# Performance work log

Measured on AMD Instinct MI355X. Metric: run time of the kernel, lower is better.

The kernel has to match this reference:

```python
import jax, jax.numpy as jnp
import numpy as np

N = 262144
IN_DIM = 64
HID = 256
EMB = 128
OUT = 64
B = 16
MAX_AISLES = 64
NUM_SEG = B * MAX_AISLES  # static upper bound on number of (batch, aisle) segments


def setup_inputs() -> dict:
    key = jax.random.key(0)
    ks = jax.random.split(key, 16)
    def lin(k, fan_in, fan_out):
        bound = 1.0 / np.sqrt(fan_in)
        kw, kb = jax.random.split(k)
        W = jax.random.uniform(kw, (fan_in, fan_out), jnp.float32, -bound, bound)
        b = jax.random.uniform(kb, (fan_out,), jnp.float32, -bound, bound)
        return W, b
    W1, b1 = lin(ks[0], IN_DIM, HID)
    W2, b2 = lin(ks[1], HID, HID)
    W3, b3 = lin(ks[2], HID, EMB)
    A1, c1 = lin(ks[3], 2 * EMB, HID)
    A2, c2 = lin(ks[4], HID, HID)
    A3, c3 = lin(ks[5], HID, OUT)
    x = jax.random.normal(ks[6], (N, IN_DIM), jnp.float32)
    aisle_nrs = jax.random.randint(ks[7], (N,), 0, MAX_AISLES, jnp.int32)
    batch = jnp.sort(jax.random.randint(ks[8], (N,), 0, B, jnp.int32))
    return {"x": x, "aisle_nrs": aisle_nrs, "batch": batch,
            "W1": W1, "b1": b1, "W2": W2, "b2": b2, "W3": W3, "b3": b3,
            "A1": A1, "c1": c1, "A2": A2, "c2": c2, "A3": A3, "c3": c3}


def reference(x, aisle_nrs, batch, W1, b1, W2, b2, W3, b3, A1, c1, A2, c2, A3, c3):
    lrelu = lambda v: jax.nn.leaky_relu(v, 0.01)  # torch LeakyReLU default slope
    h = lrelu(x @ W1 + b1)
    h = lrelu(h @ W2 + b2)
    h = h @ W3 + b3  # [N, EMB]
    # dynamic group id: aisle + batch * (max_aisle + 1)
    aisle_ids = aisle_nrs + batch * (jnp.max(aisle_nrs) + 1)
    # scatter-mean over segments (NUM_SEG is a static upper bound)
    sums = jax.ops.segment_sum(h, aisle_ids, num_segments=NUM_SEG)
    counts = jax.ops.segment_sum(jnp.ones((h.shape[0],), h.dtype), aisle_ids,
                                 num_segments=NUM_SEG)
    means = sums / jnp.maximum(counts, 1.0)[:, None]
    # gather back and concat
    z = jnp.concatenate([h, means[aisle_ids]], axis=1)  # [N, 2*EMB]
    z = lrelu(z @ A1 + c1)
    z = lrelu(z @ A2 + c2)
    z = z @ A3 + c3
    return z
```

## Files before the change

### kernel.cpp

```cpp
#include <hip/hip_runtime.h>
#include <hip/hip_bf16.h>

#define N_ROWS 262144
#define IN_DIM 64
#define HID 256
#define EMB 128
#define OUT_DIM 64
#define NSEG 1024
#define ROWS_B 128
#define MT 8
#define NWAVE 8
#define LDS_S 264
#define CHUNK 1024
#define NSLOTS (2 * (N_ROWS / CHUNK))

typedef _Float16 h16;
typedef _Float16 h16x8 __attribute__((ext_vector_type(8)));
typedef _Float16 h16x4 __attribute__((ext_vector_type(4)));
typedef float f32x4 __attribute__((ext_vector_type(4)));


__global__ void k_max(const int* __restrict__ aisle, int* __restrict__ maxA) {
    int v = 0;
    for (int i = blockIdx.x * blockDim.x + threadIdx.x; i < N_ROWS; i += gridDim.x * blockDim.x)
        v = max(v, aisle[i]);
#pragma unroll
    for (int off = 32; off > 0; off >>= 1) v = max(v, __shfl_down(v, off));
    __shared__ int red[4];
    if ((threadIdx.x & 63) == 0) red[threadIdx.x >> 6] = v;
    __syncthreads();
    if (threadIdx.x == 0) {
        int m = red[0];
        for (int i = 1; i < 4; ++i) m = max(m, red[i]);
        atomicMax(maxA, m);
    }
}

__device__ __forceinline__ void frag_nk(int o, int K, int& n, int& k) {
    int tile = o / (16 * K);
    int r = o - tile * 16 * K;
    n = tile * 16 + ((r >> 3) & 15);
    k = (r >> 9) * 32 + (((r >> 7) & 3) << 3) + (r & 7);
}

__global__ void k_prep_weights(const float* __restrict__ W1, const float* __restrict__ W2,
                               const float* __restrict__ W3, const float* __restrict__ A1f,
                               const float* __restrict__ A2f, const float* __restrict__ A3f,
                               h16* __restrict__ W1t, h16* __restrict__ W2t, h16* __restrict__ W3t,
                               h16* __restrict__ A1t, h16* __restrict__ A2t, h16* __restrict__ A3t) {
    int idx = blockIdx.x * 256 + threadIdx.x;
    int n, k;
    if (idx < 16384)       { int o = idx;          frag_nk(o, 64, n, k);  W1t[o] = (h16)W1[k * 256 + n]; }
    else if (idx < 81920)  { int o = idx - 16384;  frag_nk(o, 256, n, k); W2t[o] = (h16)W2[k * 256 + n]; }
    else if (idx < 114688) { int o = idx - 81920;  frag_nk(o, 256, n, k); W3t[o] = (h16)W3[k * 128 + n]; }
    else if (idx < 180224) { int o = idx - 114688; frag_nk(o, 256, n, k); A1t[o] = (h16)A1f[k * 256 + n]; }
    else if (idx < 245760) { int o = idx - 180224; frag_nk(o, 256, n, k); A2t[o] = (h16)A2f[k * 256 + n]; }
    else                   { int o = idx - 245760; frag_nk(o, 256, n, k); A3t[o] = (h16)A3f[k * 64  + n]; }
}

template <int K, int NOUT, bool ACT>
__device__ __forceinline__ void mlp_layer_ip(const h16* __restrict__ Wt,
                                             const float* __restrict__ bias,
                                             h16* __restrict__ S,
                                             int lane, int wave) {
    constexpr int NW = NOUT / NWAVE;
    constexpr int NT = NW / 16;
    constexpr int KT = K / 32;
    const int l15 = lane & 15, l4 = lane >> 4;
    f32x4 acc[MT][NT];
#pragma unroll
    for (int mt = 0; mt < MT; ++mt)
#pragma unroll
        for (int nt = 0; nt < NT; ++nt)
#pragma unroll
            for (int j = 0; j < 4; ++j) acc[mt][nt][j] = 0.f;

    const h16* wb[NT];
#pragma unroll
    for (int nt = 0; nt < NT; ++nt)
        wb[nt] = Wt + (size_t)(wave * NT + nt) * 16 * K + lane * 8;

    h16x8 b0[NT], b1[NT], b2[NT];
#pragma unroll
    for (int nt = 0; nt < NT; ++nt) b0[nt] = *(const h16x8*)wb[nt];
    if (KT > 1) {
#pragma unroll
        for (int nt = 0; nt < NT; ++nt) b1[nt] = *(const h16x8*)(wb[nt] + 512);
    }
    if (KT > 2) {
#pragma unroll
        for (int nt = 0; nt < NT; ++nt) b2[nt] = *(const h16x8*)(wb[nt] + 1024);
    }

#pragma unroll
    for (int kt = 0; kt < KT; ++kt) {
        h16x8 bc[NT];
#pragma unroll
        for (int nt = 0; nt < NT; ++nt) bc[nt] = b0[nt];
#pragma unroll
        for (int nt = 0; nt < NT; ++nt) b0[nt] = b1[nt];
#pragma unroll
        for (int nt = 0; nt < NT; ++nt) b1[nt] = b2[nt];
        if (kt + 3 < KT) {
#pragma unroll
            for (int nt = 0; nt < NT; ++nt) b2[nt] = *(const h16x8*)(wb[nt] + (kt + 3) * 512);
        }
        __builtin_amdgcn_s_setprio(1);
#pragma unroll
        for (int mt = 0; mt < MT; ++mt) {
            h16x8 a = *(const h16x8*)&S[(mt * 16 + l15) * LDS_S + kt * 32 + l4 * 8];
#pragma unroll
            for (int nt = 0; nt < NT; ++nt)
                acc[mt][nt] = __builtin_amdgcn_mfma_f32_16x16x32_f16(bc[nt], a, acc[mt][nt], 0, 0, 0);
        }
        __builtin_amdgcn_s_setprio(0);
    }

    __syncthreads();

#pragma unroll
    for (int nt = 0; nt < NT; ++nt) {
        const int cb = wave * NW + nt * 16 + l4 * 4;
        const f32x4 bias4 = *(const f32x4*)&bias[cb];
#pragma unroll
        for (int mt = 0; mt < MT; ++mt) {
            f32x4 v = acc[mt][nt] + bias4;
            if (ACT) {
#pragma unroll
                for (int j = 0; j < 4; ++j) v[j] = fmaxf(v[j], 0.01f * v[j]);
            }
            h16x4 hv;
#pragma unroll
            for (int j = 0; j < 4; ++j) hv[j] = (h16)v[j];
            *(h16x4*)&S[(mt * 16 + l15) * LDS_S + cb] = hv;
        }
    }
    __syncthreads();
}

__device__ __forceinline__ void mlp_layer_out_h16(const h16* __restrict__ Wt,
                                                  const float* __restrict__ bias,
                                                  const h16* __restrict__ S,
                                                  h16* __restrict__ gout, int row0,
                                                  int lane, int wave) {
    const int l15 = lane & 15, l4 = lane >> 4;
    f32x4 acc[MT];
#pragma unroll
    for (int mt = 0; mt < MT; ++mt)
#pragma unroll
        for (int j = 0; j < 4; ++j) acc[mt][j] = 0.f;

    const h16* wb = Wt + (size_t)wave * 16 * 256 + lane * 8;
    h16x8 b0 = *(const h16x8*)wb;
    h16x8 b1 = *(const h16x8*)(wb + 512);
    h16x8 b2 = *(const h16x8*)(wb + 1024);
#pragma unroll
    for (int kt = 0; kt < 8; ++kt) {
        h16x8 bc = b0;
        b0 = b1;
        b1 = b2;
        if (kt + 3 < 8) b2 = *(const h16x8*)(wb + (kt + 3) * 512);
        __builtin_amdgcn_s_setprio(1);
#pragma unroll
        for (int mt = 0; mt < MT; ++mt) {
            h16x8 a = *(const h16x8*)&S[(mt * 16 + l15) * LDS_S + kt * 32 + l4 * 8];
            acc[mt] = __builtin_amdgcn_mfma_f32_16x16x32_f16(bc, a, acc[mt], 0, 0, 0);
        }
        __builtin_amdgcn_s_setprio(0);
    }

    const int cb = wave * 16 + l4 * 4;
    const f32x4 bias4 = *(const f32x4*)&bias[cb];
#pragma unroll
    for (int mt = 0; mt < MT; ++mt) {
        f32x4 v = acc[mt] + bias4;
        h16x4 hv;
#pragma unroll
        for (int j = 0; j < 4; ++j) hv[j] = (h16)v[j];
        *(h16x4*)&gout[(size_t)(row0 + mt * 16 + l15) * 128 + cb] = hv;
    }
}

__global__ __launch_bounds__(512, 4) void k1(const float* __restrict__ x,
                                             const h16* __restrict__ W1t, const float* __restrict__ b1,
                                             const h16* __restrict__ W2t, const float* __restrict__ b2,
                                             const h16* __restrict__ W3t, const float* __restrict__ b3,
                                             h16* __restrict__ hbuf) {
    __shared__ __align__(16) h16 S[ROWS_B * LDS_S];
    const int tid = threadIdx.x, lane = tid & 63, wave = tid >> 6;
    const int row0 = blockIdx.x * ROWS_B;

    {
        const int r = tid >> 2, c16 = (tid & 3) * 16;
        const float* src = &x[(size_t)(row0 + r) * 64 + c16];
        f32x4 v0 = *(const f32x4*)&src[0];
        f32x4 v1 = *(const f32x4*)&src[4];
        f32x4 v2 = *(const f32x4*)&src[8];
        f32x4 v3 = *(const f32x4*)&src[12];
        h16x8 h0, h1;
#pragma unroll
        for (int j = 0; j < 4; ++j) { h0[j] = (h16)v0[j]; h0[4 + j] = (h16)v1[j];
                                      h1[j] = (h16)v2[j]; h1[4 + j] = (h16)v3[j]; }
        *(h16x8*)&S[r * LDS_S + c16]     = h0;
        *(h16x8*)&S[r * LDS_S + c16 + 8] = h1;
    }
    __syncthreads();

    mlp_layer_ip<64, 256, true>(W1t, b1, S, lane, wave);
    mlp_layer_ip<256, 256, true>(W2t, b2, S, lane, wave);
    mlp_layer_out_h16(W3t, b3, S, hbuf, row0, lane, wave);
}

__global__ __launch_bounds__(256) void k_scatter(const h16* __restrict__ hbuf,
                                                 const int* __restrict__ aisle,
                                                 const int* __restrict__ batch,
                                                 float* __restrict__ partials,
                                                 float* __restrict__ pcount,
                                                 int* __restrict__ bvmap) {
    __shared__ int la[CHUNK], lb[CHUNK], rankv[CHUNK], rowlist[CHUNK];
    __shared__ int hist[128], scan[128];
    const int tid = threadIdx.x;
    const int row0 = blockIdx.x * CHUNK;

    if (tid < 128) hist[tid] = 0;
    for (int i = tid; i < CHUNK; i += 256) { la[i] = aisle[row0 + i]; lb[i] = batch[row0 + i]; }
    __syncthreads();

    const int bLo = lb[0], bHi = lb[CHUNK - 1];

    for (int i = tid; i < CHUNK; i += 256) {
        int slot = min(lb[i] - bLo, 1);
        rankv[i] = atomicAdd(&hist[slot * 64 + la[i]], 1);
    }
    __syncthreads();
    if (tid < 128) scan[tid] = hist[tid];
    __syncthreads();
#pragma unroll
    for (int st = 1; st < 128; st <<= 1) {
        int v = 0;
        if (tid < 128 && tid >= st) v = scan[tid - st];
        __syncthreads();
        if (tid < 128) scan[tid] += v;
        __syncthreads();
    }
    for (int i = tid; i < CHUNK; i += 256) {
        int bin = min(lb[i] - bLo, 1) * 64 + la[i];
        rowlist[scan[bin] - hist[bin] + rankv[i]] = i;
    }
    __syncthreads();

    const int a_own = tid >> 2, cg = tid & 3;
    for (int slot = 0; slot < 2; ++slot) {
        const int sid = blockIdx.x * 2 + slot;
        const int bv = bLo + slot;
        if (bv > bHi) { if (tid == 0) bvmap[sid] = -1; continue; }

        const int bin = slot * 64 + a_own;
        const int s1 = scan[bin];
        const int s0 = s1 - hist[bin];

        float acc[32];
#pragma unroll
        for (int j = 0; j < 32; ++j) acc[j] = 0.f;

        for (int idx = s0; idx < s1; ++idx) {
            const int r = rowlist[idx];
            const h16x8* src = (const h16x8*)&hbuf[(size_t)(row0 + r) * 128 + cg * 32];
            h16x8 v0 = src[0], v1 = src[1], v2 = src[2], v3 = src[3];
#pragma unroll
            for (int j = 0; j < 8; ++j) {
                acc[j]      += (float)v0[j];
                acc[8 + j]  += (float)v1[j];
                acc[16 + j] += (float)v2[j];
                acc[24 + j] += (float)v3[j];
            }
        }
        float* dst = &partials[(size_t)sid * 8192 + tid * 32];
#pragma unroll
        for (int g2 = 0; g2 < 8; ++g2) *(f32x4*)&dst[g2 * 4] = *(const f32x4*)&acc[g2 * 4];
        if (cg == 0) pcount[sid * 64 + a_own] = (float)(s1 - s0);
        if (tid == 0) bvmap[sid] = bv;
    }
}

__global__ __launch_bounds__(128) void k_means(const float* __restrict__ partials,
                                               const float* __restrict__ pcount,
                                               const int* __restrict__ bvmap,
                                               h16* __restrict__ means,
                                               const int* __restrict__ maxA) {
    __shared__ int sbv[NSLOTS];
    const int b = blockIdx.x >> 6, a = blockIdx.x & 63;
    const int tid = threadIdx.x;
    const int mult = *maxA + 1;
    for (int i = tid; i < NSLOTS; i += 128) sbv[i] = bvmap[i];
    __syncthreads();
    if (a >= mult) return;

    float sum = 0.f, cnt = 0.f;
    for (int s = 0; s < NSLOTS; ++s) {
        if (sbv[s] == b) {
            sum += partials[(size_t)s * 8192 + a * 128 + tid];
            cnt += pcount[s * 64 + a];
        }
    }
    means[(size_t)(b * mult + a) * 128 + tid] = (h16)(sum / fmaxf(cnt, 1.0f));
}

__global__ __launch_bounds__(512, 4) void k3(const h16* __restrict__ hbuf,
                                             const int* __restrict__ aisle,
                                             const int* __restrict__ batch,
                                             const h16* __restrict__ means,
                                             const h16* __restrict__ A1t, const float* __restrict__ c1,
                                             const h16* __restrict__ A2t, const float* __restrict__ c2,
                                             const h16* __restrict__ A3t, const float* __restrict__ c3,
                                             float* __restrict__ out, const int* __restrict__ maxA) {
    __shared__ __align__(16) h16 S[ROWS_B * LDS_S];
    const int tid = threadIdx.x, lane = tid & 63, wave = tid >> 6;
    const int row0 = blockIdx.x * ROWS_B;
    const int mult = *maxA + 1;

    {
        const int r = tid >> 2, p = tid & 3;
        const int g = row0 + r;
        const h16x8* hs = (const h16x8*)&hbuf[(size_t)g * 128 + p * 32];
        h16x8* hd = (h16x8*)&S[r * LDS_S + p * 32];
        hd[0] = hs[0]; hd[1] = hs[1]; hd[2] = hs[2]; hd[3] = hs[3];
        const int id = aisle[g] + batch[g] * mult;
        const h16x8* ms = (const h16x8*)&means[(size_t)id * 128 + p * 32];
        h16x8* md = (h16x8*)&S[r * LDS_S + 128 + p * 32];
        md[0] = ms[0]; md[1] = ms[1]; md[2] = ms[2]; md[3] = ms[3];
    }
    __syncthreads();

    mlp_layer_ip<256, 256, true>(A1t, c1, S, lane, wave);
    mlp_layer_ip<256, 256, true>(A2t, c2, S, lane, wave);

    {
        const int l15 = lane & 15, l4 = lane >> 4;
        const int w4 = wave & 3, kw = wave >> 2;
        f32x4 acc4[MT];
#pragma unroll
        for (int mt = 0; mt < MT; ++mt)
#pragma unroll
            for (int j = 0; j < 4; ++j) acc4[mt][j] = 0.f;

        const h16* wb = A3t + (size_t)w4 * 16 * 256 + (size_t)kw * 4 * 512 + lane * 8;
        h16x8 b0 = *(const h16x8*)wb;
        h16x8 b1 = *(const h16x8*)(wb + 512);
        h16x8 b2 = *(const h16x8*)(wb + 1024);
#pragma unroll
        for (int kt = 0; kt < 4; ++kt) {
            h16x8 bc = b0;
            b0 = b1;
            b1 = b2;
            if (kt + 3 < 4) b2 = *(const h16x8*)(wb + (kt + 3) * 512);
            __builtin_amdgcn_s_setprio(1);
#pragma unroll
            for (int mt = 0; mt < MT; ++mt) {
                h16x8 a = *(const h16x8*)&S[(mt * 16 + l15) * LDS_S + kw * 128 + kt * 32 + l4 * 8];
                acc4[mt] = __builtin_amdgcn_mfma_f32_16x16x32_f16(bc, a, acc4[mt], 0, 0, 0);
            }
            __builtin_amdgcn_s_setprio(0);
        }
        __syncthreads();
        float* fS = (float*)S;
        if (kw == 1) {
#pragma unroll
            for (int mt = 0; mt < MT; ++mt) {
                const int row = mt * 16 + l15;
                *(f32x4*)&fS[row * 68 + w4 * 16 + l4 * 4] = acc4[mt];
            }
        }
        __syncthreads();
        if (kw == 0) {
            const f32x4 bias4 = *(const f32x4*)&c3[w4 * 16 + l4 * 4];
#pragma unroll
            for (int mt = 0; mt < MT; ++mt) {
                const int row = mt * 16 + l15;
                f32x4 p = *(const f32x4*)&fS[row * 68 + w4 * 16 + l4 * 4];
                f32x4 v = acc4[mt] + p + bias4;
                *(f32x4*)&out[(size_t)(row0 + row) * 64 + w4 * 16 + l4 * 4] = v;
            }
        }
    }
}

extern "C" void kernel_launch(void* const* d_in, const int* in_sizes, int n_in,
                              void* d_out, int out_size, void* d_ws, size_t ws_size,
                              hipStream_t stream) {
    const float* x     = (const float*)d_in[0];
    const int*   aisle = (const int*)d_in[1];
    const int*   batch = (const int*)d_in[2];
    const float* W1 = (const float*)d_in[3];  const float* b1 = (const float*)d_in[4];
    const float* W2 = (const float*)d_in[5];  const float* b2 = (const float*)d_in[6];
    const float* W3 = (const float*)d_in[7];  const float* b3 = (const float*)d_in[8];
    const float* A1 = (const float*)d_in[9];  const float* c1 = (const float*)d_in[10];
    const float* A2 = (const float*)d_in[11]; const float* c2 = (const float*)d_in[12];
    const float* A3 = (const float*)d_in[13]; const float* c3 = (const float*)d_in[14];
    float* out = (float*)d_out;

    char* w = (char*)d_ws;
    size_t off = 0;
    h16*   hbuf     = (h16*)(w + off);   off += (size_t)N_ROWS * 128 * sizeof(h16);
    float* partials = (float*)(w + off); off += (size_t)NSLOTS * 8192 * sizeof(float);
    float* pcount   = (float*)(w + off); off += NSLOTS * 64 * sizeof(float);
    int*   bvmap    = (int*)(w + off);   off += NSLOTS * sizeof(int);
    h16*   means    = (h16*)(w + off);   off += NSEG * 128 * sizeof(h16);
    h16*   W1t      = (h16*)(w + off);   off += 16384 * sizeof(h16);
    h16*   W2t      = (h16*)(w + off);   off += 65536 * sizeof(h16);
    h16*   W3t      = (h16*)(w + off);   off += 32768 * sizeof(h16);
    h16*   A1t      = (h16*)(w + off);   off += 65536 * sizeof(h16);
    h16*   A2t      = (h16*)(w + off);   off += 65536 * sizeof(h16);
    h16*   A3t      = (h16*)(w + off);   off += 16384 * sizeof(h16);
    int*   maxA     = (int*)(w + off);   off += 256;

    hipMemsetAsync(maxA, 0, sizeof(int), stream);

    k_max<<<256, 256, 0, stream>>>(aisle, maxA);
    k_prep_weights<<<1024, 256, 0, stream>>>(W1, W2, W3, A1, A2, A3, W1t, W2t, W3t, A1t, A2t, A3t);
    k1<<<N_ROWS / ROWS_B, 512, 0, stream>>>(x, W1t, b1, W2t, b2, W3t, b3, hbuf);
    k_scatter<<<N_ROWS / CHUNK, 256, 0, stream>>>(hbuf, aisle, batch, partials, pcount, bvmap);
    k_means<<<16 * 64, 128, 0, stream>>>(partials, pcount, bvmap, means, maxA);
    k3<<<N_ROWS / ROWS_B, 512, 0, stream>>>(hbuf, aisle, batch, means, A1t, c1, A2t, c2, A3t, c3,
                                            out, maxA);
}
```

Before: 341.6 us.

## Fuse max into weight prep, widen scatter blocks, bound means slot scan

```diff
diff --git a/kernel.cpp b/kernel.cpp
--- a/kernel.cpp
+++ b/kernel.cpp
@@ -19,43 +19,35 @@
 typedef _Float16 h16x4 __attribute__((ext_vector_type(4)));
 typedef float f32x4 __attribute__((ext_vector_type(4)));
 
-
-__global__ void k_max(const int* __restrict__ aisle, int* __restrict__ maxA) {
-    int v = 0;
-    for (int i = blockIdx.x * blockDim.x + threadIdx.x; i < N_ROWS; i += gridDim.x * blockDim.x)
-        v = max(v, aisle[i]);
+__device__ __forceinline__ int frag_off(int k, int n) {
+    return ((k >> 5) << 9) + (((k >> 3) & 3) << 7) + ((n & 15) << 3) + (k & 7);
+}
+
+__global__ __launch_bounds__(256) void k_prep(const float* __restrict__ W1, const float* __restrict__ W2,
+                                              const float* __restrict__ W3, const float* __restrict__ A1f,
+                                              const float* __restrict__ A2f, const float* __restrict__ A3f,
+                                              const int* __restrict__ aisle, int* __restrict__ maxA,
+                                              h16* __restrict__ W1t, h16* __restrict__ W2t, h16* __restrict__ W3t,
+                                              h16* __restrict__ A1t, h16* __restrict__ A2t, h16* __restrict__ A3t) {
+    const int idx = blockIdx.x * 256 + threadIdx.x;
+
+    int v = aisle[idx];
 #pragma unroll
     for (int off = 32; off > 0; off >>= 1) v = max(v, __shfl_down(v, off));
-    __shared__ int red[4];
-    if ((threadIdx.x & 63) == 0) red[threadIdx.x >> 6] = v;
-    __syncthreads();
-    if (threadIdx.x == 0) {
-        int m = red[0];
-        for (int i = 1; i < 4; ++i) m = max(m, red[i]);
-        atomicMax(maxA, m);
-    }
-}
-
-__device__ __forceinline__ void frag_nk(int o, int K, int& n, int& k) {
-    int tile = o / (16 * K);
-    int r = o - tile * 16 * K;
-    n = tile * 16 + ((r >> 3) & 15);
-    k = (r >> 9) * 32 + (((r >> 7) & 3) << 3) + (r & 7);
-}
-
-__global__ void k_prep_weights(const float* __restrict__ W1, const float* __restrict__ W2,
-                               const float* __restrict__ W3, const float* __restrict__ A1f,
-                               const float* __restrict__ A2f, const float* __restrict__ A3f,
-                               h16* __restrict__ W1t, h16* __restrict__ W2t, h16* __restrict__ W3t,
-                               h16* __restrict__ A1t, h16* __restrict__ A2t, h16* __restrict__ A3t) {
-    int idx = blockIdx.x * 256 + threadIdx.x;
-    int n, k;
-    if (idx < 16384)       { int o = idx;          frag_nk(o, 64, n, k);  W1t[o] = (h16)W1[k * 256 + n]; }
-    else if (idx < 81920)  { int o = idx - 16384;  frag_nk(o, 256, n, k); W2t[o] = (h16)W2[k * 256 + n]; }
-    else if (idx < 114688) { int o = idx - 81920;  frag_nk(o, 256, n, k); W3t[o] = (h16)W3[k * 128 + n]; }
-    else if (idx < 180224) { int o = idx - 114688; frag_nk(o, 256, n, k); A1t[o] = (h16)A1f[k * 256 + n]; }
-    else if (idx < 245760) { int o = idx - 180224; frag_nk(o, 256, n, k); A2t[o] = (h16)A2f[k * 256 + n]; }
-    else                   { int o = idx - 245760; frag_nk(o, 256, n, k); A3t[o] = (h16)A3f[k * 64  + n]; }
+    if ((threadIdx.x & 63) == 0) atomicMax(maxA, v);
+
+    if (idx < 16384)       { int i = idx;          int k = i >> 8, n = i & 255;
+                             W1t[((n >> 4) << 10) + frag_off(k, n)] = (h16)W1[i]; }
+    else if (idx < 81920)  { int i = idx - 16384;  int k = i >> 8, n = i & 255;
+                             W2t[((n >> 4) << 12) + frag_off(k, n)] = (h16)W2[i]; }
+    else if (idx < 114688) { int i = idx - 81920;  int k = i >> 7, n = i & 127;
+                             W3t[((n >> 4) << 12) + frag_off(k, n)] = (h16)W3[i]; }
+    else if (idx < 180224) { int i = idx - 114688; int k = i >> 8, n = i & 255;
+                             A1t[((n >> 4) << 12) + frag_off(k, n)] = (h16)A1f[i]; }
+    else if (idx < 245760) { int i = idx - 180224; int k = i >> 8, n = i & 255;
+                             A2t[((n >> 4) << 12) + frag_off(k, n)] = (h16)A2f[i]; }
+    else                   { int i = idx - 245760; int k = i >> 6, n = i & 63;
+                             A3t[((n >> 4) << 12) + frag_off(k, n)] = (h16)A3f[i]; }
 }
 
 template <int K, int NOUT, bool ACT>
@@ -211,26 +203,27 @@
     mlp_layer_out_h16(W3t, b3, S, hbuf, row0, lane, wave);
 }
 
-__global__ __launch_bounds__(256) void k_scatter(const h16* __restrict__ hbuf,
-                                                 const int* __restrict__ aisle,
-                                                 const int* __restrict__ batch,
-                                                 float* __restrict__ partials,
-                                                 float* __restrict__ pcount,
-                                                 int* __restrict__ bvmap) {
+__global__ __launch_bounds__(1024) void k_scatter(const h16* __restrict__ hbuf,
+                                                  const int* __restrict__ aisle,
+                                                  const int* __restrict__ batch,
+                                                  float* __restrict__ partials,
+                                                  float* __restrict__ pcount,
+                                                  int* __restrict__ bvmap) {
     __shared__ int la[CHUNK], lb[CHUNK], rankv[CHUNK], rowlist[CHUNK];
     __shared__ int hist[128], scan[128];
     const int tid = threadIdx.x;
     const int row0 = blockIdx.x * CHUNK;
 
     if (tid < 128) hist[tid] = 0;
-    for (int i = tid; i < CHUNK; i += 256) { la[i] = aisle[row0 + i]; lb[i] = batch[row0 + i]; }
+    la[tid] = aisle[row0 + tid];
+    lb[tid] = batch[row0 + tid];
     __syncthreads();
 
     const int bLo = lb[0], bHi = lb[CHUNK - 1];
 
-    for (int i = tid; i < CHUNK; i += 256) {
-        int slot = min(lb[i] - bLo, 1);
-        rankv[i] = atomicAdd(&hist[slot * 64 + la[i]], 1);
+    {
+        int slot = min(lb[tid] - bLo, 1);
+        rankv[tid] = atomicAdd(&hist[slot * 64 + la[tid]], 1);
     }
     __syncthreads();
     if (tid < 128) scan[tid] = hist[tid];
@@ -243,43 +236,41 @@
         if (tid < 128) scan[tid] += v;
         __syncthreads();
     }
-    for (int i = tid; i < CHUNK; i += 256) {
-        int bin = min(lb[i] - bLo, 1) * 64 + la[i];
-        rowlist[scan[bin] - hist[bin] + rankv[i]] = i;
-    }
-    __syncthreads();
-
-    const int a_own = tid >> 2, cg = tid & 3;
-    for (int slot = 0; slot < 2; ++slot) {
-        const int sid = blockIdx.x * 2 + slot;
-        const int bv = bLo + slot;
-        if (bv > bHi) { if (tid == 0) bvmap[sid] = -1; continue; }
-
+    {
+        int bin = min(lb[tid] - bLo, 1) * 64 + la[tid];
+        rowlist[scan[bin] - hist[bin] + rankv[tid]] = tid;
+    }
+    __syncthreads();
+
+    const int slot = tid >> 9;
+    const int sub  = tid & 511;
+    const int a_own = sub >> 3, cg = sub & 7;
+    const int sid = blockIdx.x * 2 + slot;
+    const int bv = bLo + slot;
+    if (sub == 0) bvmap[sid] = (bv <= bHi) ? bv : -1;
+    if (bv <= bHi) {
         const int bin = slot * 64 + a_own;
         const int s1 = scan[bin];
         const int s0 = s1 - hist[bin];
 
-        float acc[32];
-#pragma unroll
-        for (int j = 0; j < 32; ++j) acc[j] = 0.f;
+        float acc[16];
+#pragma unroll
+        for (int j = 0; j < 16; ++j) acc[j] = 0.f;
 
         for (int idx = s0; idx < s1; ++idx) {
             const int r = rowlist[idx];
-            const h16x8* src = (const h16x8*)&hbuf[(size_t)(row0 + r) * 128 + cg * 32];
-            h16x8 v0 = src[0], v1 = src[1], v2 = src[2], v3 = src[3];
+            const h16x8* src = (const h16x8*)&hbuf[(size_t)(row0 + r) * 128 + cg * 16];
+            h16x8 v0 = src[0], v1 = src[1];
 #pragma unroll
             for (int j = 0; j < 8; ++j) {
-                acc[j]      += (float)v0[j];
-                acc[8 + j]  += (float)v1[j];
-                acc[16 + j] += (float)v2[j];
-                acc[24 + j] += (float)v3[j];
+                acc[j]     += (float)v0[j];
+                acc[8 + j] += (float)v1[j];
             }
         }
-        float* dst = &partials[(size_t)sid * 8192 + tid * 32];
-#pragma unroll
-        for (int g2 = 0; g2 < 8; ++g2) *(f32x4*)&dst[g2 * 4] = *(const f32x4*)&acc[g2 * 4];
+        float* dst = &partials[(size_t)sid * 8192 + a_own * 128 + cg * 16];
+#pragma unroll
+        for (int g2 = 0; g2 < 4; ++g2) *(f32x4*)&dst[g2 * 4] = *(const f32x4*)&acc[g2 * 4];
         if (cg == 0) pcount[sid * 64 + a_own] = (float)(s1 - s0);
-        if (tid == 0) bvmap[sid] = bv;
     }
 }
 
@@ -289,15 +280,26 @@
                                                h16* __restrict__ means,
                                                const int* __restrict__ maxA) {
     __shared__ int sbv[NSLOTS];
+    __shared__ int lohi[2];
     const int b = blockIdx.x >> 6, a = blockIdx.x & 63;
     const int tid = threadIdx.x;
     const int mult = *maxA + 1;
     for (int i = tid; i < NSLOTS; i += 128) sbv[i] = bvmap[i];
+    if (tid == 0) { lohi[0] = NSLOTS; lohi[1] = 0; }
+    __syncthreads();
+    int llo = NSLOTS, lhi = 0;
+#pragma unroll
+    for (int q = 0; q < 4; ++q) {
+        const int i = tid * 4 + q;
+        if (sbv[i] == b) { if (i < llo) llo = i; lhi = i + 1; }
+    }
+    if (llo < NSLOTS) atomicMin(&lohi[0], llo);
+    if (lhi > 0)      atomicMax(&lohi[1], lhi);
     __syncthreads();
     if (a >= mult) return;
 
     float sum = 0.f, cnt = 0.f;
-    for (int s = 0; s < NSLOTS; ++s) {
+    for (int s = lohi[0]; s < lohi[1]; ++s) {
         if (sbv[s] == b) {
             sum += partials[(size_t)s * 8192 + a * 128 + tid];
             cnt += pcount[s * 64 + a];
@@ -416,10 +418,10 @@
 
     hipMemsetAsync(maxA, 0, sizeof(int), stream);
 
-    k_max<<<256, 256, 0, stream>>>(aisle, maxA);
-    k_prep_weights<<<1024, 256, 0, stream>>>(W1, W2, W3, A1, A2, A3, W1t, W2t, W3t, A1t, A2t, A3t);
+    k_prep<<<1024, 256, 0, stream>>>(W1, W2, W3, A1, A2, A3, aisle, maxA,
+                                     W1t, W2t, W3t, A1t, A2t, A3t);
     k1<<<N_ROWS / ROWS_B, 512, 0, stream>>>(x, W1t, b1, W2t, b2, W3t, b3, hbuf);
-    k_scatter<<<N_ROWS / CHUNK, 256, 0, stream>>>(hbuf, aisle, batch, partials, pcount, bvmap);
+    k_scatter<<<N_ROWS / CHUNK, 1024, 0, stream>>>(hbuf, aisle, batch, partials, pcount, bvmap);
     k_means<<<16 * 64, 128, 0, stream>>>(partials, pcount, bvmap, means, maxA);
     k3<<<N_ROWS / ROWS_B, 512, 0, stream>>>(hbuf, aisle, batch, means, A1t, c1, A2t, c2, A3t, c3,
                                             out, maxA);
```

Measured after the change: 352.0 us. 1.03x slower.

## Halve waves per block so each wave computes more output columns

Applied to the files above, without the earlier changes.

```diff
diff --git a/kernel.cpp b/kernel.cpp
--- a/kernel.cpp
+++ b/kernel.cpp
@@ -9,7 +9,7 @@
 #define NSEG 1024
 #define ROWS_B 128
 #define MT 8
-#define NWAVE 8
+#define NWAVE 4
 #define LDS_S 264
 #define CHUNK 1024
 #define NSLOTS (2 * (N_ROWS / CHUNK))
@@ -144,44 +144,64 @@
                                                   h16* __restrict__ gout, int row0,
                                                   int lane, int wave) {
     const int l15 = lane & 15, l4 = lane >> 4;
-    f32x4 acc[MT];
+    f32x4 acc[MT][2];
 #pragma unroll
     for (int mt = 0; mt < MT; ++mt)
 #pragma unroll
-        for (int j = 0; j < 4; ++j) acc[mt][j] = 0.f;
-
-    const h16* wb = Wt + (size_t)wave * 16 * 256 + lane * 8;
-    h16x8 b0 = *(const h16x8*)wb;
-    h16x8 b1 = *(const h16x8*)(wb + 512);
-    h16x8 b2 = *(const h16x8*)(wb + 1024);
+        for (int nt = 0; nt < 2; ++nt)
+#pragma unroll
+            for (int j = 0; j < 4; ++j) acc[mt][nt][j] = 0.f;
+
+    const h16* wb[2];
+#pragma unroll
+    for (int nt = 0; nt < 2; ++nt)
+        wb[nt] = Wt + (size_t)(wave * 2 + nt) * 16 * 256 + lane * 8;
+
+    h16x8 b0[2], b1[2], b2[2];
+#pragma unroll
+    for (int nt = 0; nt < 2; ++nt) { b0[nt] = *(const h16x8*)wb[nt];
+                                     b1[nt] = *(const h16x8*)(wb[nt] + 512);
+                                     b2[nt] = *(const h16x8*)(wb[nt] + 1024); }
 #pragma unroll
     for (int kt = 0; kt < 8; ++kt) {
-        h16x8 bc = b0;
-        b0 = b1;
-        b1 = b2;
-        if (kt + 3 < 8) b2 = *(const h16x8*)(wb + (kt + 3) * 512);
+        h16x8 bc[2];
+#pragma unroll
+        for (int nt = 0; nt < 2; ++nt) bc[nt] = b0[nt];
+#pragma unroll
+        for (int nt = 0; nt < 2; ++nt) b0[nt] = b1[nt];
+#pragma unroll
+        for (int nt = 0; nt < 2; ++nt) b1[nt] = b2[nt];
+        if (kt + 3 < 8) {
+#pragma unroll
+            for (int nt = 0; nt < 2; ++nt) b2[nt] = *(const h16x8*)(wb[nt] + (kt + 3) * 512);
+        }
         __builtin_amdgcn_s_setprio(1);
 #pragma unroll
         for (int mt = 0; mt < MT; ++mt) {
             h16x8 a = *(const h16x8*)&S[(mt * 16 + l15) * LDS_S + kt * 32 + l4 * 8];
-            acc[mt] = __builtin_amdgcn_mfma_f32_16x16x32_f16(bc, a, acc[mt], 0, 0, 0);
+#pragma unroll
+            for (int nt = 0; nt < 2; ++nt)
+                acc[mt][nt] = __builtin_amdgcn_mfma_f32_16x16x32_f16(bc[nt], a, acc[mt][nt], 0, 0, 0);
         }
         __builtin_amdgcn_s_setprio(0);
     }
 
-    const int cb = wave * 16 + l4 * 4;
-    const f32x4 bias4 = *(const f32x4*)&bias[cb];
-#pragma unroll
-    for (int mt = 0; mt < MT; ++mt) {
-        f32x4 v = acc[mt] + bias4;
-        h16x4 hv;
-#pragma unroll
-        for (int j = 0; j < 4; ++j) hv[j] = (h16)v[j];
-        *(h16x4*)&gout[(size_t)(row0 + mt * 16 + l15) * 128 + cb] = hv;
-    }
-}
-
-__global__ __launch_bounds__(512, 4) void k1(const float* __restrict__ x,
+#pragma unroll
+    for (int nt = 0; nt < 2; ++nt) {
+        const int cb = wave * 32 + nt * 16 + l4 * 4;
+        const f32x4 bias4 = *(const f32x4*)&bias[cb];
+#pragma unroll
+        for (int mt = 0; mt < MT; ++mt) {
+            f32x4 v = acc[mt][nt] + bias4;
+            h16x4 hv;
+#pragma unroll
+            for (int j = 0; j < 4; ++j) hv[j] = (h16)v[j];
+            *(h16x4*)&gout[(size_t)(row0 + mt * 16 + l15) * 128 + cb] = hv;
+        }
+    }
+}
+
+__global__ __launch_bounds__(256, 2) void k1(const float* __restrict__ x,
                                              const h16* __restrict__ W1t, const float* __restrict__ b1,
                                              const h16* __restrict__ W2t, const float* __restrict__ b2,
                                              const h16* __restrict__ W3t, const float* __restrict__ b3,
@@ -190,8 +210,8 @@
     const int tid = threadIdx.x, lane = tid & 63, wave = tid >> 6;
     const int row0 = blockIdx.x * ROWS_B;
 
-    {
-        const int r = tid >> 2, c16 = (tid & 3) * 16;
+    for (int i = tid; i < 512; i += 256) {
+        const int r = i >> 2, c16 = (i & 3) * 16;
         const float* src = &x[(size_t)(row0 + r) * 64 + c16];
         f32x4 v0 = *(const f32x4*)&src[0];
         f32x4 v1 = *(const f32x4*)&src[4];
@@ -306,7 +326,7 @@
     means[(size_t)(b * mult + a) * 128 + tid] = (h16)(sum / fmaxf(cnt, 1.0f));
 }
 
-__global__ __launch_bounds__(512, 4) void k3(const h16* __restrict__ hbuf,
+__global__ __launch_bounds__(256, 2) void k3(const h16* __restrict__ hbuf,
                                              const int* __restrict__ aisle,
                                              const int* __restrict__ batch,
                                              const h16* __restrict__ means,
@@ -319,8 +339,8 @@
     const int row0 = blockIdx.x * ROWS_B;
     const int mult = *maxA + 1;
 
-    {
-        const int r = tid >> 2, p = tid & 3;
+    for (int i = tid; i < 512; i += 256) {
+        const int r = i >> 2, p = i & 3;
         const int g = row0 + r;
         const h16x8* hs = (const h16x8*)&hbuf[(size_t)g * 128 + p * 32];
         h16x8* hd = (h16x8*)&S[r * LDS_S + p * 32];
@@ -337,50 +357,35 @@
 
     {
         const int l15 = lane & 15, l4 = lane >> 4;
-        const int w4 = wave & 3, kw = wave >> 2;
         f32x4 acc4[MT];
 #pragma unroll
         for (int mt = 0; mt < MT; ++mt)
 #pragma unroll
             for (int j = 0; j < 4; ++j) acc4[mt][j] = 0.f;
 
-        const h16* wb = A3t + (size_t)w4 * 16 * 256 + (size_t)kw * 4 * 512 + lane * 8;
+        const h16* wb = A3t + (size_t)wave * 16 * 256 + lane * 8;
         h16x8 b0 = *(const h16x8*)wb;
         h16x8 b1 = *(const h16x8*)(wb + 512);
         h16x8 b2 = *(const h16x8*)(wb + 1024);
 #pragma unroll
-        for (int kt = 0; kt < 4; ++kt) {
+        for (int kt = 0; kt < 8; ++kt) {
             h16x8 bc = b0;
             b0 = b1;
             b1 = b2;
-            if (kt + 3 < 4) b2 = *(const h16x8*)(wb + (kt + 3) * 512);
+            if (kt + 3 < 8) b2 = *(const h16x8*)(wb + (kt + 3) * 512);
             __builtin_amdgcn_s_setprio(1);
 #pragma unroll
             for (int mt = 0; mt < MT; ++mt) {
-                h16x8 a = *(const h16x8*)&S[(mt * 16 + l15) * LDS_S + kw * 128 + kt * 32 + l4 * 8];
+                h16x8 a = *(const h16x8*)&S[(mt * 16 + l15) * LDS_S + kt * 32 + l4 * 8];
                 acc4[mt] = __builtin_amdgcn_mfma_f32_16x16x32_f16(bc, a, acc4[mt], 0, 0, 0);
             }
             __builtin_amdgcn_s_setprio(0);
         }
-        __syncthreads();
-        float* fS = (float*)S;
-        if (kw == 1) {
-#pragma unroll
-            for (int mt = 0; mt < MT; ++mt) {
-                const int row = mt * 16 + l15;
-                *(f32x4*)&fS[row * 68 + w4 * 16 + l4 * 4] = acc4[mt];
-            }
-        }
-        __syncthreads();
-        if (kw == 0) {
-            const f32x4 bias4 = *(const f32x4*)&c3[w4 * 16 + l4 * 4];
-#pragma unroll
-            for (int mt = 0; mt < MT; ++mt) {
-                const int row = mt * 16 + l15;
-                f32x4 p = *(const f32x4*)&fS[row * 68 + w4 * 16 + l4 * 4];
-                f32x4 v = acc4[mt] + p + bias4;
-                *(f32x4*)&out[(size_t)(row0 + row) * 64 + w4 * 16 + l4 * 4] = v;
-            }
+        const f32x4 bias4 = *(const f32x4*)&c3[wave * 16 + l4 * 4];
+#pragma unroll
+        for (int mt = 0; mt < MT; ++mt) {
+            f32x4 v = acc4[mt] + bias4;
+            *(f32x4*)&out[(size_t)(row0 + mt * 16 + l15) * 64 + wave * 16 + l4 * 4] = v;
         }
     }
 }
@@ -418,9 +423,9 @@
 
     k_max<<<256, 256, 0, stream>>>(aisle, maxA);
     k_prep_weights<<<1024, 256, 0, stream>>>(W1, W2, W3, A1, A2, A3, W1t, W2t, W3t, A1t, A2t, A3t);
-    k1<<<N_ROWS / ROWS_B, 512, 0, stream>>>(x, W1t, b1, W2t, b2, W3t, b3, hbuf);
+    k1<<<N_ROWS / ROWS_B, 256, 0, stream>>>(x, W1t, b1, W2t, b2, W3t, b3, hbuf);
     k_scatter<<<N_ROWS / CHUNK, 256, 0, stream>>>(hbuf, aisle, batch, partials, pcount, bvmap);
     k_means<<<16 * 64, 128, 0, stream>>>(partials, pcount, bvmap, means, maxA);
-    k3<<<N_ROWS / ROWS_B, 512, 0, stream>>>(hbuf, aisle, batch, means, A1t, c1, A2t, c2, A3t, c3,
+    k3<<<N_ROWS / ROWS_B, 256, 0, stream>>>(hbuf, aisle, batch, means, A1t, c1, A2t, c2, A3t, c3,
                                             out, maxA);
 }
```

Result: slower. 354.4 us (+3.7%).
